# Kernel tuning notes

Measured on AMD Instinct MI355X. Metric: run time of the kernel, lower is better.

The kernel has to match this reference:

```python
import jax, jax.numpy as jnp
import numpy as np
import math

D_MODEL = 1024
NUM_HEADS = 16
D_K = D_MODEL // NUM_HEADS


def setup_inputs() -> dict:
    key = jax.random.key(0)
    ks = jax.random.split(key, 7)
    B, S = 2, 2048
    scale = 1.0 / math.sqrt(D_MODEL)
    inp = {
        "q": jax.random.normal(ks[0], (B, S, D_MODEL), dtype=jnp.float32),
        "k": jax.random.normal(ks[1], (B, S, D_MODEL), dtype=jnp.float32),
        "v": jax.random.normal(ks[2], (B, S, D_MODEL), dtype=jnp.float32),
        # Source module reuses q_linear for q, k, and v projections, so only
        # Wq/bq are needed for the input projections; out projection separate.
        "Wq": jax.random.normal(ks[3], (D_MODEL, D_MODEL), dtype=jnp.float32) * scale,
        "bq": jnp.zeros((D_MODEL,), dtype=jnp.float32),
        "Wo": jax.random.normal(ks[4], (D_MODEL, D_MODEL), dtype=jnp.float32) * scale,
        "bo": jnp.zeros((D_MODEL,), dtype=jnp.float32),
    }
    return inp


def _attention(q, k, v, Wq, bq, Wo, bo):
    B, S, _ = q.shape

    def proj(x):
        # [B,S,D] -> [B,H,S,d_k]
        y = jnp.einsum("bsd,de->bse", x, Wq) + bq
        return y.reshape(B, S, NUM_HEADS, D_K).transpose(0, 2, 1, 3)

    qh, kh, vh = proj(q), proj(k), proj(v)
    # scores: [B,H,S,S]
    scores = jnp.einsum("bhsd,bhtd->bhst", qh, kh) / math.sqrt(D_K)
    attn = jax.nn.softmax(scores, axis=-1)
    # dropout: eval-mode identity
    out = jnp.einsum("bhst,bhtd->bhsd", attn, vh)  # [B,H,S,d_k]
    out = out.transpose(0, 2, 1, 3).reshape(B, S, D_MODEL)
    return jnp.einsum("bsd,de->bse", out, Wo) + bo


def reference(q, k, v, Wq, bq, Wo, bo):
    return _attention(q, k, v, Wq, bq, Wo, bo)
```

## Files before the change

kernel.cpp:

```cpp
#include <hip/hip_runtime.h>
#include <hip/hip_bf16.h>

typedef unsigned short u16;
typedef unsigned int   u32;
typedef __attribute__((ext_vector_type(8))) short bf16x8;
typedef __attribute__((ext_vector_type(4))) float f32x4;
typedef __attribute__((ext_vector_type(16))) float f32x16;

#define SEQ     2048
#define DM      1024
#define NH      16
#define DKH     64
#define PER_SRC 4194304

#define OFF_VT   0u
#define OFF_AOH  8388608u
#define OFF_WQT  25165824u
#define OFF_WOT  27262976u
#define OFF_QH   29360128u
#define OFF_KH   37748736u
#define OFF_VH   46137344u
#define OFF_PML  46137344u
#define OFF_PO   54525952u
#define NEED_WS  71303168u
#define PART_O_U 4194304
#define PART_ML_F 131072

__device__ __forceinline__ u16 f2bf(float f) {
    union { float f; u32 u; } c; c.f = f;
    return (u16)((c.u + 0x7fffu + ((c.u >> 16) & 1u)) >> 16);
}

__device__ __forceinline__ float bf2f(u16 h) {
    union { u32 u; float f; } c; c.u = (u32)h << 16;
    return c.f;
}

__device__ __forceinline__ u32 cvt_pk_bf16(float lo, float hi) {
    u32 r;
    asm("v_cvt_pk_bf16_f32 %0, %1, %2" : "=v"(r) : "v"(lo), "v"(hi));
    return r;
}

__device__ __forceinline__ void gload_lds16(const void* g, void* l) {
    __builtin_amdgcn_global_load_lds((__attribute__((address_space(1))) void*)g,
                                     (__attribute__((address_space(3))) void*)l,
                                     16, 0, 0);
}

__global__ void prep(const float* __restrict__ q, const float* __restrict__ k,
                     const float* __restrict__ v, const float* __restrict__ Wq,
                     const float* __restrict__ Wo, u16* __restrict__ xb,
                     u16* __restrict__ Wqt, u16* __restrict__ Wot) {
    int bid = blockIdx.x;
    int tid = threadIdx.x;
    if (bid < 6144) {
        int srcid = bid >> 11;
        const float* src = (srcid == 0) ? q : (srcid == 1) ? k : v;
        u16* dst = xb + (size_t)srcid * PER_SRC;
        size_t i = ((size_t)(bid & 2047) * 256 + tid) * 8;
        float4 a = *(const float4*)(src + i);
        float4 b = *(const float4*)(src + i + 4);
        bf16x8 o;
        o[0] = (short)f2bf(a.x); o[1] = (short)f2bf(a.y);
        o[2] = (short)f2bf(a.z); o[3] = (short)f2bf(a.w);
        o[4] = (short)f2bf(b.x); o[5] = (short)f2bf(b.y);
        o[6] = (short)f2bf(b.z); o[7] = (short)f2bf(b.w);
        *(bf16x8*)(dst + i) = o;
    } else {
        int b2 = bid - 6144;
        const float* W = (b2 >= 256) ? Wo : Wq;
        u16* Wt       = (b2 >= 256) ? Wot : Wqt;
        int bx = b2 & 255;
        int k0 = (bx & 15) * 64;
        int n0 = (bx >> 4) * 64;
        __shared__ __align__(16) float t[64][68];
        int r = tid >> 2, cs = (tid & 3) * 16;
        #pragma unroll
        for (int j = 0; j < 4; ++j) {
            float4 vv = *(const float4*)(W + (size_t)(k0 + r) * DM + n0 + cs + j * 4);
            *(float4*)&t[r][cs + j * 4] = vv;
        }
        __syncthreads();
        bf16x8 o0, o1;
        #pragma unroll
        for (int j = 0; j < 8; ++j) o0[j] = (short)f2bf(t[cs + j][r]);
        #pragma unroll
        for (int j = 0; j < 8; ++j) o1[j] = (short)f2bf(t[cs + 8 + j][r]);
        u16* dst = Wt + (size_t)(n0 + r) * DM + k0 + cs;
        *(bf16x8*)(dst)     = o0;
        *(bf16x8*)(dst + 8) = o1;
    }
}

__global__ void vtrans(const u16* __restrict__ vh, u16* __restrict__ vt) {
    int bh = blockIdx.y, st = blockIdx.x;
    __shared__ u16 t[64][72];
    int tid = threadIdx.x;
    int r = tid >> 2, cs = (tid & 3) * 16;
    const u16* src = vh + ((size_t)bh * SEQ + st * 64 + r) * DKH + cs;
    bf16x8 v0 = *(const bf16x8*)(src);
    bf16x8 v1 = *(const bf16x8*)(src + 8);
    #pragma unroll
    for (int j = 0; j < 8; ++j) { t[r][cs + j] = (u16)v0[j]; t[r][cs + 8 + j] = (u16)v1[j]; }
    __syncthreads();
    bf16x8 o0, o1;
    #pragma unroll
    for (int j = 0; j < 8; ++j) o0[j] = (short)t[cs + j][r];
    #pragma unroll
    for (int j = 0; j < 8; ++j) o1[j] = (short)t[cs + 8 + j][r];
    bf16x8 w0, w1;
    #pragma unroll
    for (int j = 0; j < 4; ++j) {
        w0[j] = o0[j];     w0[4 + j] = o1[j];
        w1[j] = o0[4 + j]; w1[4 + j] = o1[4 + j];
    }
    u16* dst = vt + ((size_t)bh * DKH + r) * SEQ + st * 64 + cs;
    *(bf16x8*)(dst)     = w0;
    *(bf16x8*)(dst + 8) = w1;
}

__global__ __launch_bounds__(256)
void gemm_qkv(const u16* __restrict__ Abase, const u16* __restrict__ Bt,
              const float* __restrict__ bias, u16* __restrict__ outbase)
{
    __shared__ __align__(16) u16 Alds[128 * 64];
    __shared__ __align__(16) u16 Blds[128 * 64];

    const int tid  = threadIdx.x;
    const int wave = tid >> 6;
    const int lane = tid & 63;
    const int low4 = lane & 15;
    const int quad = lane >> 4;
    const int bid  = blockIdx.x;
    const int xcd  = bid & 7;
    const int j    = bid >> 3;
    const int m0 = (xcd * 4 + (j >> 3)) * 128;
    const int n0 = (j & 7) * 128;
    const int wm = (wave >> 1) * 64, wn = (wave & 1) * 64;

    const u16* A = Abase + (size_t)blockIdx.z * PER_SRC;

    f32x4 acc[4][4] = {};

    for (int kt = 0; kt < DM / 64; ++kt) {
        #pragma unroll
        for (int it = 0; it < 4; ++it) {
            int seg  = it * 256 + tid;
            int row  = seg >> 3;
            int slot = seg & 7;
            int ss   = slot ^ (row & 7);
            gload_lds16(A + (size_t)(m0 + row) * DM + kt * 64 + ss * 8,
                        &Alds[(it * 256 + wave * 64) * 8]);
            gload_lds16(Bt + (size_t)(n0 + row) * DM + kt * 64 + ss * 8,
                        &Blds[(it * 256 + wave * 64) * 8]);
        }
        __syncthreads();
        #pragma unroll
        for (int kk = 0; kk < 2; ++kk) {
            bf16x8 af[4], bfr[4];
            #pragma unroll
            for (int mi = 0; mi < 4; ++mi) {
                int row = wm + mi * 16 + low4;
                af[mi] = *(const bf16x8*)&Alds[row * 64 + (((kk * 4 + quad) ^ (row & 7)) * 8)];
            }
            #pragma unroll
            for (int ni = 0; ni < 4; ++ni) {
                int row = wn + ni * 16 + low4;
                bfr[ni] = *(const bf16x8*)&Blds[row * 64 + (((kk * 4 + quad) ^ (row & 7)) * 8)];
            }
            #pragma unroll
            for (int mi = 0; mi < 4; ++mi)
                #pragma unroll
                for (int ni = 0; ni < 4; ++ni)
                    acc[mi][ni] = __builtin_amdgcn_mfma_f32_16x16x32_bf16(
                        af[mi], bfr[ni], acc[mi][ni], 0, 0, 0);
        }
        __syncthreads();
    }

    #pragma unroll
    for (int mi = 0; mi < 4; ++mi) {
        #pragma unroll
        for (int ni = 0; ni < 4; ++ni) {
            int n = n0 + wn + ni * 16 + low4;
            float bv = bias[n];
            #pragma unroll
            for (int j2 = 0; j2 < 4; ++j2) {
                int m = m0 + wm + mi * 16 + quad * 4 + j2;
                float val = acc[mi][ni][j2] + bv;
                u16* dst = outbase + (size_t)blockIdx.z * PER_SRC;
                int b = m >> 11, s = m & (SEQ - 1);
                int h = n >> 6, dd = n & 63;
                dst[(size_t)(b * NH + h) * (SEQ * DKH) + (size_t)s * DKH + dd] = f2bf(val);
            }
        }
    }
}

template<int MERGE>
__global__ __launch_bounds__(256)
void gemm_o(const u16* __restrict__ Abf, const u16* __restrict__ pOb,
            const float* __restrict__ pml, const u16* __restrict__ Bt,
            const float* __restrict__ bias, float* __restrict__ out)
{
    __shared__ __align__(16) u16 Alds[64 * 64];
    __shared__ __align__(16) u16 Blds[128 * 64];
    __shared__ __align__(16) float wlds[NH * 64 * 2];

    const int tid  = threadIdx.x;
    const int wave = tid >> 6;
    const int lane = tid & 63;
    const int low4 = lane & 15;
    const int quad = lane >> 4;
    const int bid  = blockIdx.x;
    const int xcd  = bid & 7;
    const int j    = bid >> 3;
    const int m0 = (xcd * 8 + (j >> 3)) * 64;
    const int n0 = (j & 7) * 128;
    const int wm = (wave >> 1) * 32, wn = (wave & 1) * 64;

    const int b      = m0 >> 11;
    const int s_base = m0 & (SEQ - 1);

    if (MERGE == 1) {
        #pragma unroll
        for (int idx = tid; idx < NH * 64; idx += 256) {
            int h  = idx >> 6;
            int sl = idx & 63;
            size_t row = (((size_t)(b * NH + h)) << 11) + s_base + sl;
            float2 ml1 = *(const float2*)&pml[row * 2];
            float2 ml2 = *(const float2*)&pml[PART_ML_F + row * 2];
            float m  = fmaxf(ml1.x, ml2.x);
            float w1 = __builtin_amdgcn_exp2f(ml1.x - m);
            float w2 = __builtin_amdgcn_exp2f(ml2.x - m);
            float inv = 1.0f / (ml1.y * w1 + ml2.y * w2);
            wlds[idx * 2]     = w1 * inv;
            wlds[idx * 2 + 1] = w2 * inv;
        }
        __syncthreads();
    }

    f32x4 acc[2][4] = {};

    for (int kt = 0; kt < DM / 64; ++kt) {
        #pragma unroll
        for (int it = 0; it < 2; ++it) {
            int seg  = it * 256 + tid;
            int row  = seg >> 3;
            int slot = seg & 7;
            int ss   = slot ^ (row & 7);
            size_t arow = (((size_t)(b * NH + kt)) << 11) + s_base + row;
            if (MERGE == 0) {
                gload_lds16(Abf + arow * DKH + ss * 8, &Alds[seg * 8]);
            } else {
                const u16* s1 = pOb + arow * DKH + ss * 8;
                const u16* s2 = s1 + PART_O_U;
                bf16x8 x = *(const bf16x8*)s1;
                bf16x8 y = *(const bf16x8*)s2;
                float a1 = wlds[(kt * 64 + row) * 2];
                float a2 = wlds[(kt * 64 + row) * 2 + 1];
                uint4 pv;
                pv.x = cvt_pk_bf16(bf2f((u16)x[0]) * a1 + bf2f((u16)y[0]) * a2,
                                   bf2f((u16)x[1]) * a1 + bf2f((u16)y[1]) * a2);
                pv.y = cvt_pk_bf16(bf2f((u16)x[2]) * a1 + bf2f((u16)y[2]) * a2,
                                   bf2f((u16)x[3]) * a1 + bf2f((u16)y[3]) * a2);
                pv.z = cvt_pk_bf16(bf2f((u16)x[4]) * a1 + bf2f((u16)y[4]) * a2,
                                   bf2f((u16)x[5]) * a1 + bf2f((u16)y[5]) * a2);
                pv.w = cvt_pk_bf16(bf2f((u16)x[6]) * a1 + bf2f((u16)y[6]) * a2,
                                   bf2f((u16)x[7]) * a1 + bf2f((u16)y[7]) * a2);
                *(uint4*)&Alds[seg * 8] = pv;
            }
        }
        #pragma unroll
        for (int it = 0; it < 4; ++it) {
            int seg  = it * 256 + tid;
            int row  = seg >> 3;
            int slot = seg & 7;
            int ss   = slot ^ (row & 7);
            gload_lds16(Bt + (size_t)(n0 + row) * DM + kt * 64 + ss * 8,
                        &Blds[seg * 8]);
        }
        __syncthreads();
        #pragma unroll
        for (int kk = 0; kk < 2; ++kk) {
            bf16x8 af[2], bfr[4];
            #pragma unroll
            for (int mi = 0; mi < 2; ++mi) {
                int row = wm + mi * 16 + low4;
                af[mi] = *(const bf16x8*)&Alds[row * 64 + (((kk * 4 + quad) ^ (row & 7)) * 8)];
            }
            #pragma unroll
            for (int ni = 0; ni < 4; ++ni) {
                int row = wn + ni * 16 + low4;
                bfr[ni] = *(const bf16x8*)&Blds[row * 64 + (((kk * 4 + quad) ^ (row & 7)) * 8)];
            }
            #pragma unroll
            for (int mi = 0; mi < 2; ++mi)
                #pragma unroll
                for (int ni = 0; ni < 4; ++ni)
                    acc[mi][ni] = __builtin_amdgcn_mfma_f32_16x16x32_bf16(
                        af[mi], bfr[ni], acc[mi][ni], 0, 0, 0);
        }
        __syncthreads();
    }

    #pragma unroll
    for (int mi = 0; mi < 2; ++mi) {
        #pragma unroll
        for (int ni = 0; ni < 4; ++ni) {
            int n = n0 + wn + ni * 16 + low4;
            float bv = bias[n];
            #pragma unroll
            for (int j2 = 0; j2 < 4; ++j2) {
                int m = m0 + wm + mi * 16 + quad * 4 + j2;
                out[(size_t)m * DM + n] = acc[mi][ni][j2] + bv;
            }
        }
    }
}

template<int SPLIT>
__global__ __launch_bounds__(256, 2)
void attn(const u16* __restrict__ qh, const u16* __restrict__ kh,
          const u16* __restrict__ vt, u16* __restrict__ aoh,
          u16* __restrict__ pOb, float* __restrict__ pml)
{
    __shared__ __align__(16) u16 lds[2][8192];

    const int tid  = threadIdx.x;
    const int w    = tid >> 6;
    const int lane = tid & 63;
    const int l31  = lane & 31;
    const int hi   = lane >> 5;

    int bid = blockIdx.x;
    int lid = (bid & 7) * 64 + (bid >> 3);
    const int qt = lid & 15;
    const int bh = lid >> 4;
    const int part = SPLIT ? blockIdx.y : 0;
    const int kt0  = SPLIT ? part * 16 : 0;
    const int nkt  = SPLIT ? 16 : 32;

    const int qbase = qt * 128 + w * 32;
    const int q_row = qbase + l31;

    const float SC = 0.18033688f;

    bf16x8 qf[4];
    #pragma unroll
    for (int c = 0; c < 4; ++c)
        qf[c] = *(const bf16x8*)&qh[((size_t)bh * SEQ + q_row) * DKH + c * 16 + hi * 8];

    float m_r = -1e30f, l_r = 0.f;
    f32x16 ot[2] = {};

#define STAGE(buf, kt_)                                                                 \
    {                                                                                   \
        _Pragma("unroll")                                                               \
        for (int it = 0; it < 2; ++it) {                                                \
            int seg  = it * 256 + tid;                                                  \
            int row  = seg >> 3;                                                        \
            int slot = seg & 7;                                                         \
            int ss   = slot ^ (row & 7);                                                \
            gload_lds16(kh + ((size_t)bh * SEQ + (kt_) * 64 + row) * DKH + ss * 8,      \
                        &lds[buf][(it * 256 + w * 64) * 8]);                            \
            gload_lds16(vt + ((size_t)bh * DKH + row) * SEQ + (kt_) * 64 + ss * 8,      \
                        &lds[buf][4096 + (it * 256 + w * 64) * 8]);                     \
        }                                                                               \
    }

    STAGE(0, kt0);
    __syncthreads();

    int cur = 0;
    for (int ki = 0; ki < nkt; ++ki) {
        if (ki + 1 < nkt) STAGE(cur ^ 1, kt0 + ki + 1);

        const u16* Klds = &lds[cur][0];
        const u16* Vlds = &lds[cur][4096];

        f32x16 st[2];
        #pragma unroll
        for (int T = 0; T < 2; ++T) {
            f32x16 acc = {};
            __builtin_amdgcn_s_setprio(1);
            #pragma unroll
            for (int c = 0; c < 4; ++c) {
                int row = T * 32 + l31;
                bf16x8 kf = *(const bf16x8*)&Klds[row * 64 + (((c * 2 + hi) ^ (row & 7)) * 8)];
                acc = __builtin_amdgcn_mfma_f32_32x32x16_bf16(kf, qf[c], acc, 0, 0, 0);
            }
            __builtin_amdgcn_s_setprio(0);
            st[T] = acc;
        }

        float mx[8];
        #pragma unroll
        for (int r = 0; r < 8; ++r)
            mx[r] = fmaxf(fmaxf(st[0][r], st[0][r + 8]),
                          fmaxf(st[1][r], st[1][r + 8]));
        float t0 = fmaxf(fmaxf(mx[0], mx[1]), mx[2]);
        float t1 = fmaxf(fmaxf(mx[3], mx[4]), mx[5]);
        float t2 = fmaxf(mx[6], mx[7]);
        float lmax = fmaxf(fmaxf(t0, t1), t2);
        float mloc = fmaxf(lmax, __shfl_xor(lmax, 32)) * SC;

        float mnew = fmaxf(m_r, mloc);
        if (!__all(mloc <= m_r + 11.5f)) {
            float fac = __builtin_amdgcn_exp2f(m_r - mnew);
            m_r = mnew;
            l_r *= fac;
            #pragma unroll
            for (int dt = 0; dt < 2; ++dt)
                #pragma unroll
                for (int r = 0; r < 16; ++r) ot[dt][r] *= fac;
        }

        float nm = -m_r;
        float rs0 = 0.f, rs1 = 0.f, rs2 = 0.f, rs3 = 0.f;
        #pragma unroll
        for (int T = 0; T < 2; ++T)
            #pragma unroll
            for (int r = 0; r < 16; r += 4) {
                float p0 = __builtin_amdgcn_exp2f(fmaf(st[T][r],     SC, nm));
                float p1 = __builtin_amdgcn_exp2f(fmaf(st[T][r + 1], SC, nm));
                float p2 = __builtin_amdgcn_exp2f(fmaf(st[T][r + 2], SC, nm));
                float p3 = __builtin_amdgcn_exp2f(fmaf(st[T][r + 3], SC, nm));
                st[T][r] = p0; st[T][r + 1] = p1; st[T][r + 2] = p2; st[T][r + 3] = p3;
                rs0 += p0; rs1 += p1; rs2 += p2; rs3 += p3;
            }
        float rsum = (rs0 + rs1) + (rs2 + rs3);
        l_r += rsum + __shfl_xor(rsum, 32);

        u32 pk[2][8];
        #pragma unroll
        for (int T = 0; T < 2; ++T)
            #pragma unroll
            for (int g = 0; g < 8; ++g)
                pk[T][g] = cvt_pk_bf16(st[T][2 * g], st[T][2 * g + 1]);

        __builtin_amdgcn_s_setprio(1);
        #pragma unroll
        for (int dt = 0; dt < 2; ++dt)
            #pragma unroll
            for (int c = 0; c < 4; ++c) {
                int row = dt * 32 + l31;
                bf16x8 vf = *(const bf16x8*)&Vlds[row * 64 + (((c * 2 + hi) ^ (row & 7)) * 8)];
                union { bf16x8 v; u32 u[4]; } pf;
                int T = c >> 1, g0 = (c & 1) * 4;
                pf.u[0] = pk[T][g0];     pf.u[1] = pk[T][g0 + 1];
                pf.u[2] = pk[T][g0 + 2]; pf.u[3] = pk[T][g0 + 3];
                ot[dt] = __builtin_amdgcn_mfma_f32_32x32x16_bf16(vf, pf.v, ot[dt], 0, 0, 0);
            }
        __builtin_amdgcn_s_setprio(0);

        __syncthreads();
        cur ^= 1;
    }

    float inv = (SPLIT == 0) ? (1.0f / l_r) : 1.0f;
    u16* dstb = (SPLIT == 0) ? aoh : (pOb + (size_t)part * PART_O_U);
    u16* tile = &lds[0][0] + w * 2048;
    #pragma unroll
    for (int dt = 0; dt < 2; ++dt)
        #pragma unroll
        for (int g = 0; g < 4; ++g) {
            u32 w0 = cvt_pk_bf16(ot[dt][4 * g] * inv,     ot[dt][4 * g + 1] * inv);
            u32 w1 = cvt_pk_bf16(ot[dt][4 * g + 2] * inv, ot[dt][4 * g + 3] * inv);
            int d0 = 8 * g + 4 * hi + 32 * dt;
            int byteoff = l31 * 128 + ((d0 * 2) ^ ((l31 & 7) << 4));
            uint2 pr; pr.x = w0; pr.y = w1;
            *(uint2*)((char*)tile + byteoff) = pr;
        }
    const size_t gbase = ((size_t)bh * SEQ + qbase) * DKH;
    #pragma unroll
    for (int p = 0; p < 4; ++p) {
        int q = p * 8 + (lane >> 3);
        int byteoff = q * 128 + (((lane & 7) * 16) ^ ((q & 7) << 4));
        bf16x8 val = *(const bf16x8*)((const char*)tile + byteoff);
        *(bf16x8*)&dstb[gbase + p * 512 + lane * 8] = val;
    }
    if (SPLIT == 1 && hi == 0) {
        float2 ml; ml.x = m_r; ml.y = l_r;
        *(float2*)&pml[(size_t)part * PART_ML_F + ((size_t)bh * SEQ + qbase + l31) * 2] = ml;
    }
#undef STAGE
}

extern "C" void kernel_launch(void* const* d_in, const int* in_sizes, int n_in,
                              void* d_out, int out_size, void* d_ws, size_t ws_size,
                              hipStream_t stream)
{
    const float* q  = (const float*)d_in[0];
    const float* k  = (const float*)d_in[1];
    const float* v  = (const float*)d_in[2];
    const float* Wq = (const float*)d_in[3];
    const float* bq = (const float*)d_in[4];
    const float* Wo = (const float*)d_in[5];
    const float* bo = (const float*)d_in[6];

    char* ws = (char*)d_ws;
    u16* xb  = (u16*)(ws);
    u16* wqt = (u16*)(ws + OFF_WQT);
    u16* wot = (u16*)(ws + OFF_WOT);
    u16* qh  = (u16*)(ws + OFF_QH);
    u16* kh  = (u16*)(ws + OFF_KH);
    u16* vh  = (u16*)(ws + OFF_VH);
    u16* vt  = (u16*)(ws + OFF_VT);
    u16* aoh = (u16*)(ws + OFF_AOH);
    u16* pOb = (u16*)(ws + OFF_PO);
    float* pml = (float*)(ws + OFF_PML);

    prep<<<dim3(6656), dim3(256), 0, stream>>>(q, k, v, Wq, Wo, xb, wqt, wot);
    gemm_qkv<<<dim3(256, 1, 3), dim3(256), 0, stream>>>(xb, wqt, bq, qh);
    vtrans<<<dim3(32, 32), dim3(256), 0, stream>>>(vh, vt);
    if (ws_size >= (size_t)NEED_WS) {
        attn<1><<<dim3(512, 2), dim3(256), 0, stream>>>(qh, kh, vt, aoh, pOb, pml);
        gemm_o<1><<<dim3(512), dim3(256), 0, stream>>>(aoh, pOb, pml, wot, bo, (float*)d_out);
    } else {
        attn<0><<<dim3(512), dim3(256), 0, stream>>>(qh, kh, vt, aoh, pOb, pml);
        gemm_o<0><<<dim3(512), dim3(256), 0, stream>>>(aoh, pOb, pml, wot, bo, (float*)d_out);
    }
}
```

Measured before the change: 132.6 us.

## Fuse V transpose into QKV GEMM epilogue and double attention block size

The separate vtrans kernel is removed. The QKV projection GEMM now writes V directly in transposed [bh, d, s] layout, with a sequence permutation to match the layout the attention kernel expects. The attention kernel also moves to 512-thread blocks covering 256 query rows, so each staged K/V tile is shared by twice as many waves and each thread does one staging load instead of two. This saves a launch and a read/write pass over V, but the transposed stores in the GEMM epilogue are strided and uncoalesced. The larger blocks may also lower occupancy or register headroom, and the workspace grows to hold vt separately.

```diff
diff --git a/kernel.cpp b/kernel.cpp
--- a/kernel.cpp
+++ b/kernel.cpp
@@ -13,16 +13,15 @@
 #define DKH     64
 #define PER_SRC 4194304
 
-#define OFF_VT   0u
 #define OFF_AOH  8388608u
 #define OFF_WQT  25165824u
 #define OFF_WOT  27262976u
 #define OFF_QH   29360128u
 #define OFF_KH   37748736u
-#define OFF_VH   46137344u
 #define OFF_PML  46137344u
 #define OFF_PO   54525952u
-#define NEED_WS  71303168u
+#define OFF_VT   71303168u
+#define NEED_WS  79691776u
 #define PART_O_U 4194304
 #define PART_ML_F 131072
 
@@ -93,36 +92,10 @@
     }
 }
 
-__global__ void vtrans(const u16* __restrict__ vh, u16* __restrict__ vt) {
-    int bh = blockIdx.y, st = blockIdx.x;
-    __shared__ u16 t[64][72];
-    int tid = threadIdx.x;
-    int r = tid >> 2, cs = (tid & 3) * 16;
-    const u16* src = vh + ((size_t)bh * SEQ + st * 64 + r) * DKH + cs;
-    bf16x8 v0 = *(const bf16x8*)(src);
-    bf16x8 v1 = *(const bf16x8*)(src + 8);
-    #pragma unroll
-    for (int j = 0; j < 8; ++j) { t[r][cs + j] = (u16)v0[j]; t[r][cs + 8 + j] = (u16)v1[j]; }
-    __syncthreads();
-    bf16x8 o0, o1;
-    #pragma unroll
-    for (int j = 0; j < 8; ++j) o0[j] = (short)t[cs + j][r];
-    #pragma unroll
-    for (int j = 0; j < 8; ++j) o1[j] = (short)t[cs + 8 + j][r];
-    bf16x8 w0, w1;
-    #pragma unroll
-    for (int j = 0; j < 4; ++j) {
-        w0[j] = o0[j];     w0[4 + j] = o1[j];
-        w1[j] = o0[4 + j]; w1[4 + j] = o1[4 + j];
-    }
-    u16* dst = vt + ((size_t)bh * DKH + r) * SEQ + st * 64 + cs;
-    *(bf16x8*)(dst)     = w0;
-    *(bf16x8*)(dst + 8) = w1;
-}
-
 __global__ __launch_bounds__(256)
 void gemm_qkv(const u16* __restrict__ Abase, const u16* __restrict__ Bt,
-              const float* __restrict__ bias, u16* __restrict__ outbase)
+              const float* __restrict__ bias, u16* __restrict__ qkbase,
+              u16* __restrict__ vt)
 {
     __shared__ __align__(16) u16 Alds[128 * 64];
     __shared__ __align__(16) u16 Blds[128 * 64];
@@ -185,14 +158,19 @@
         for (int ni = 0; ni < 4; ++ni) {
             int n = n0 + wn + ni * 16 + low4;
             float bv = bias[n];
+            int h = n >> 6, dd = n & 63;
             #pragma unroll
             for (int j2 = 0; j2 < 4; ++j2) {
                 int m = m0 + wm + mi * 16 + quad * 4 + j2;
                 float val = acc[mi][ni][j2] + bv;
-                u16* dst = outbase + (size_t)blockIdx.z * PER_SRC;
                 int b = m >> 11, s = m & (SEQ - 1);
-                int h = n >> 6, dd = n & 63;
-                dst[(size_t)(b * NH + h) * (SEQ * DKH) + (size_t)s * DKH + dd] = f2bf(val);
+                if (blockIdx.z == 2) {
+                    int sperm = (s & ~15) | ((s & 4) << 1) | ((s & 8) >> 1) | (s & 3);
+                    vt[((size_t)(b * NH + h) * DKH + dd) * SEQ + sperm] = f2bf(val);
+                } else {
+                    u16* dst = qkbase + (size_t)blockIdx.z * PER_SRC;
+                    dst[(size_t)(b * NH + h) * (SEQ * DKH) + (size_t)s * DKH + dd] = f2bf(val);
+                }
             }
         }
     }
@@ -321,7 +299,7 @@
 }
 
 template<int SPLIT>
-__global__ __launch_bounds__(256, 2)
+__global__ __launch_bounds__(512, 2)
 void attn(const u16* __restrict__ qh, const u16* __restrict__ kh,
           const u16* __restrict__ vt, u16* __restrict__ aoh,
           u16* __restrict__ pOb, float* __restrict__ pml)
@@ -335,14 +313,14 @@
     const int hi   = lane >> 5;
 
     int bid = blockIdx.x;
-    int lid = (bid & 7) * 64 + (bid >> 3);
-    const int qt = lid & 15;
-    const int bh = lid >> 4;
+    int lid = (bid & 7) * 32 + (bid >> 3);
+    const int qt = lid & 7;
+    const int bh = lid >> 3;
     const int part = SPLIT ? blockIdx.y : 0;
     const int kt0  = SPLIT ? part * 16 : 0;
     const int nkt  = SPLIT ? 16 : 32;
 
-    const int qbase = qt * 128 + w * 32;
+    const int qbase = qt * 256 + w * 32;
     const int q_row = qbase + l31;
 
     const float SC = 0.18033688f;
@@ -357,17 +335,13 @@
 
 #define STAGE(buf, kt_)                                                                 \
     {                                                                                   \
-        _Pragma("unroll")                                                               \
-        for (int it = 0; it < 2; ++it) {                                                \
-            int seg  = it * 256 + tid;                                                  \
-            int row  = seg >> 3;                                                        \
-            int slot = seg & 7;                                                         \
-            int ss   = slot ^ (row & 7);                                                \
-            gload_lds16(kh + ((size_t)bh * SEQ + (kt_) * 64 + row) * DKH + ss * 8,      \
-                        &lds[buf][(it * 256 + w * 64) * 8]);                            \
-            gload_lds16(vt + ((size_t)bh * DKH + row) * SEQ + (kt_) * 64 + ss * 8,      \
-                        &lds[buf][4096 + (it * 256 + w * 64) * 8]);                     \
-        }                                                                               \
+        int row  = tid >> 3;                                                            \
+        int slot = tid & 7;                                                             \
+        int ss   = slot ^ (row & 7);                                                    \
+        gload_lds16(kh + ((size_t)bh * SEQ + (kt_) * 64 + row) * DKH + ss * 8,          \
+                    &lds[buf][(w * 64) * 8]);                                           \
+        gload_lds16(vt + ((size_t)bh * DKH + row) * SEQ + (kt_) * 64 + ss * 8,          \
+                    &lds[buf][4096 + (w * 64) * 8]);                                    \
     }
 
     STAGE(0, kt0);
@@ -506,20 +480,18 @@
     u16* wot = (u16*)(ws + OFF_WOT);
     u16* qh  = (u16*)(ws + OFF_QH);
     u16* kh  = (u16*)(ws + OFF_KH);
-    u16* vh  = (u16*)(ws + OFF_VH);
     u16* vt  = (u16*)(ws + OFF_VT);
     u16* aoh = (u16*)(ws + OFF_AOH);
     u16* pOb = (u16*)(ws + OFF_PO);
     float* pml = (float*)(ws + OFF_PML);
 
     prep<<<dim3(6656), dim3(256), 0, stream>>>(q, k, v, Wq, Wo, xb, wqt, wot);
-    gemm_qkv<<<dim3(256, 1, 3), dim3(256), 0, stream>>>(xb, wqt, bq, qh);
-    vtrans<<<dim3(32, 32), dim3(256), 0, stream>>>(vh, vt);
+    gemm_qkv<<<dim3(256, 1, 3), dim3(256), 0, stream>>>(xb, wqt, bq, qh, vt);
     if (ws_size >= (size_t)NEED_WS) {
-        attn<1><<<dim3(512, 2), dim3(256), 0, stream>>>(qh, kh, vt, aoh, pOb, pml);
+        attn<1><<<dim3(256, 2), dim3(512), 0, stream>>>(qh, kh, vt, aoh, pOb, pml);
         gemm_o<1><<<dim3(512), dim3(256), 0, stream>>>(aoh, pOb, pml, wot, bo, (float*)d_out);
     } else {
-        attn<0><<<dim3(512), dim3(256), 0, stream>>>(qh, kh, vt, aoh, pOb, pml);
+        attn<0><<<dim3(256), dim3(512), 0, stream>>>(qh, kh, vt, aoh, pOb, pml);
         gemm_o<0><<<dim3(512), dim3(256), 0, stream>>>(aoh, pOb, pml, wot, bo, (float*)d_out);
     }
 }
```

After: 136.2 us. 2.7% more time.
